# Performance work log

Hardware: AMD Instinct MI355X
Metric: run time of the kernel (lower is better)

The kernel has to match this reference:

```python
import jax, jax.numpy as jnp
import numpy as np


def _conv1d_same(x, k):
    # x: [N, L, Cin], k: [K, Cin, Cout] (flax Conv layout), stride 1, SAME padding
    return jax.lax.conv_general_dilated(
        x, k, window_strides=(1,), padding='SAME',
        dimension_numbers=('NWC', 'WIO', 'NWC'))


def setup_inputs() -> dict:
    key = jax.random.key(0)
    ks = jax.random.split(key, 5)
    B, T, L, C, H, OUT = 16, 64, 512, 64, 150, 24
    xs = jax.random.normal(ks[0], (B, T, L, C), jnp.float32)
    # small init scale to keep gates out of saturation
    ki = jax.random.normal(ks[1], (5, C, 3 * H), jnp.float32) * 0.05
    kh = jax.random.normal(ks[2], (5, H, 3 * H), jnp.float32) * 0.05
    W1 = jax.random.normal(ks[3], (H, H), jnp.float32) * 0.08
    b1 = jnp.zeros((H,), jnp.float32)
    W2 = jax.random.normal(ks[4], (H, OUT), jnp.float32) * 0.08
    b2 = jnp.zeros((OUT,), jnp.float32)
    return {"xs": xs, "ki": ki, "kh": kh, "W1": W1, "b1": b1, "W2": W2, "b2": b2}


def reference(xs, ki, kh, W1, b1, W2, b2):
    B, T, L, C = xs.shape
    H = kh.shape[1]
    # input-to-gates conv for all timesteps at once: [B*T, L, C] -> [B, T, L, 3H]
    gates_i = _conv1d_same(xs.reshape(B * T, L, C), ki).reshape(B, T, L, 3 * H)

    def step(h, gi):
        gh = _conv1d_same(h, kh)                      # [B, L, 3H]
        iir, iiz, iin = jnp.split(gi, 3, axis=-1)
        hir, hiz, hin = jnp.split(gh, 3, axis=-1)
        r = jax.nn.sigmoid(iir + hir)
        z = jax.nn.sigmoid(iiz + hiz)
        n = jnp.tanh(iin + r * hin)
        new_h = (1.0 - z) * n + z * h
        return new_h, new_h

    h0 = jnp.zeros((B, L, H), xs.dtype)
    _, hs = jax.lax.scan(step, h0, jnp.moveaxis(gates_i, 1, 0))  # hs: [T, B, L, H]
    last = hs[-1]                                     # out[:, -1, :] -> [B, L, H]
    hdn = last @ W1 + b1
    hdn = hdn * jax.nn.sigmoid(hdn)                   # silu
    out = hdn @ W2 + b2                               # [B, L, 24]
    return jnp.expand_dims(out, axis=-1)              # [B, L, 24, 1]
```

## Files before the change

### kernel.cpp

```cpp
#include <hip/hip_runtime.h>


#define Bn   16
#define Tn   64
#define Ln   512
#define Cn   64
#define Hn   150
#define G3   450
#define SW   160
#define HP   160
#define KCH  25
#define KCX  10
#define Mtot 8192

typedef __bf16 bf16x8 __attribute__((ext_vector_type(8)));
typedef float  f32x4  __attribute__((ext_vector_type(4)));
typedef short  s16x4  __attribute__((ext_vector_type(4)));

__device__ inline short f2bf(float f) {
  unsigned u = __builtin_bit_cast(unsigned, f);
  u += 0x7fffu + ((u >> 16) & 1u);
  return (short)(u >> 16);
}

__global__ __launch_bounds__(256) void pack_weights(const float* __restrict__ ki,
                                                    const float* __restrict__ kh,
                                                    short* __restrict__ Bx,
                                                    short* __restrict__ Bh) {
  int idx = blockIdx.x * 256 + threadIdx.x;
  if (idx < 32 * KCH * 512) {
    int j = idx & 7, lane = (idx >> 3) & 63;
    int rest = idx >> 9;
    int kc = rest % KCH, nt = rest / KCH;
    int quad = lane >> 4, l16 = lane & 15;
    int n = nt * 16 + l16, seg = n / SW, jl = n - seg * SW;
    int kk = kc / 5, jj = (kc - kk * 5) * 32 + quad * 8 + j;
    float v = (seg < 3 && jl < Hn && jj < Hn) ? kh[(kk * Hn + jj) * G3 + seg * Hn + jl] : 0.f;
    Bh[idx] = f2bf(v);
  } else {
    int r = idx - 32 * KCH * 512;
    if (r < 32 * KCX * 512) {
      int j = r & 7, lane = (r >> 3) & 63;
      int rest = r >> 9;
      int kc = rest % KCX, nt = rest / KCX;
      int quad = lane >> 4, l16 = lane & 15;
      int n = nt * 16 + l16, seg = n / SW, jl = n - seg * SW;
      int kk = kc / 2, cc = (kc - kk * 2) * 32 + quad * 8 + j;
      float v = (seg < 3 && jl < Hn) ? ki[(kk * Cn + cc) * G3 + seg * Hn + jl] : 0.f;
      Bx[r] = f2bf(v);
    }
  }
}

__global__ __launch_bounds__(640)
void gru_step(const short* __restrict__ hbin, short* __restrict__ hbout,
              float* __restrict__ hf, const short* __restrict__ Bh,
              const short* __restrict__ Bx, const float* __restrict__ xs, int t) {
  __shared__ short awh[36 * 168];
  __shared__ short awx[36 * 72];
  const int tid = threadIdx.x;
  const int bb  = blockIdx.x >> 4;
  const int l0  = (blockIdx.x & 15) * 32;

  for (int i = tid; i < 36 * 40; i += 640) {
    int r = i / 40, c4 = (i - r * 40) * 4;
    int l = l0 - 2 + r;
    s16x4 v = {0, 0, 0, 0};
    if (l >= 0 && l < Ln) v = *(const s16x4*)&hbin[((size_t)bb * Ln + l) * HP + c4];
    *(s16x4*)&awh[r * 168 + c4] = v;
  }
  for (int i = tid; i < 36 * 16; i += 640) {
    int r = i >> 4, c4 = (i & 15) * 4;
    int l = l0 - 2 + r;
    s16x4 v = {0, 0, 0, 0};
    if (l >= 0 && l < Ln) {
      f32x4 f = *(const f32x4*)&xs[(((size_t)bb * Tn + t) * Ln + l) * Cn + c4];
      v[0] = f2bf(f[0]); v[1] = f2bf(f[1]); v[2] = f2bf(f[2]); v[3] = f2bf(f[3]);
    }
    *(s16x4*)&awx[r * 72 + c4] = v;
  }
  __syncthreads();

  const int lane = tid & 63, w = tid >> 6;
  const int quad = lane >> 4, l16 = lane & 15;

  const short* Bph[3];
  const short* Bpx[3];
#pragma unroll
  for (int g = 0; g < 3; ++g) {
    Bph[g] = Bh + (size_t)(w + 10 * g) * (KCH * 512) + lane * 8;
    Bpx[g] = Bx + (size_t)(w + 10 * g) * (KCX * 512) + lane * 8;
  }
  const int arh = l16 * 168 + quad * 8;
  const int arx = l16 * 72 + quad * 8;

  f32x4 acc[2][3] = {};
  f32x4 axn[2] = {};

  bf16x8 bx[3][3];
#pragma unroll
  for (int s = 0; s < 2; ++s)
#pragma unroll
    for (int g = 0; g < 3; ++g) bx[s][g] = *(const bf16x8*)(Bpx[g] + s * 512);

  bf16x8 bh[4][3];
#pragma unroll
  for (int s = 0; s < 3; ++s)
#pragma unroll
    for (int g = 0; g < 3; ++g) bh[s][g] = *(const bf16x8*)(Bph[g] + s * 512);

#pragma unroll
  for (int kc = 0; kc < KCH; ++kc) {
    const int cur = kc & 3;
    if (kc + 3 < KCH) {
      const int nxt = (kc + 3) & 3;
#pragma unroll
      for (int g = 0; g < 3; ++g)
        bh[nxt][g] = *(const bf16x8*)(Bph[g] + (kc + 3) * 512);
    }
    const int kk = kc / 5, jj = (kc - kk * 5) * 32;
    const short* ar = &awh[arh + kk * 168 + jj];
    bf16x8 a0 = *(const bf16x8*)(ar);
    bf16x8 a1 = *(const bf16x8*)(ar + 16 * 168);
#pragma unroll
    for (int g = 0; g < 3; ++g) {
      acc[0][g] = __builtin_amdgcn_mfma_f32_16x16x32_bf16(a0, bh[cur][g], acc[0][g], 0, 0, 0);
      acc[1][g] = __builtin_amdgcn_mfma_f32_16x16x32_bf16(a1, bh[cur][g], acc[1][g], 0, 0, 0);
    }
  }

#pragma unroll
  for (int kc = 0; kc < KCX; ++kc) {
    const int cur = kc % 3;
    if (kc + 2 < KCX) {
      const int nxt = (kc + 2) % 3;
#pragma unroll
      for (int g = 0; g < 3; ++g)
        bx[nxt][g] = *(const bf16x8*)(Bpx[g] + (kc + 2) * 512);
    }
    const int kk = kc >> 1, jj = (kc & 1) * 32;
    const short* ar = &awx[arx + kk * 72 + jj];
    bf16x8 a0 = *(const bf16x8*)(ar);
    bf16x8 a1 = *(const bf16x8*)(ar + 16 * 72);
    acc[0][0] = __builtin_amdgcn_mfma_f32_16x16x32_bf16(a0, bx[cur][0], acc[0][0], 0, 0, 0);
    acc[1][0] = __builtin_amdgcn_mfma_f32_16x16x32_bf16(a1, bx[cur][0], acc[1][0], 0, 0, 0);
    acc[0][1] = __builtin_amdgcn_mfma_f32_16x16x32_bf16(a0, bx[cur][1], acc[0][1], 0, 0, 0);
    acc[1][1] = __builtin_amdgcn_mfma_f32_16x16x32_bf16(a1, bx[cur][1], acc[1][1], 0, 0, 0);
    axn[0]    = __builtin_amdgcn_mfma_f32_16x16x32_bf16(a0, bx[cur][2], axn[0], 0, 0, 0);
    axn[1]    = __builtin_amdgcn_mfma_f32_16x16x32_bf16(a1, bx[cur][2], axn[1], 0, 0, 0);
  }

  const int j = w * 16 + l16;
  if (j < Hn) {
#pragma unroll
    for (int mi = 0; mi < 2; ++mi)
#pragma unroll
      for (int r = 0; r < 4; ++r) {
        const int ml = mi * 16 + quad * 4 + r;
        const size_t mrow = (size_t)bb * Ln + l0 + ml;
        float rg = 1.f / (1.f + __expf(-acc[mi][0][r]));
        float zg = 1.f / (1.f + __expf(-acc[mi][1][r]));
        float xg = axn[mi][r] + rg * acc[mi][2][r];
        xg = fminf(fmaxf(xg, -15.f), 15.f);
        float e = __expf(2.f * xg);
        float n = (e - 1.f) / (e + 1.f);
        float hn = (1.f - zg) * n + zg * hf[mrow * Hn + j];
        hf[mrow * Hn + j] = hn;
        hbout[mrow * HP + j] = f2bf(hn);
      }
  }
}

__global__ __launch_bounds__(256) void head1(const float* __restrict__ hf,
                                             const float* __restrict__ W1,
                                             const float* __restrict__ b1,
                                             float* __restrict__ hdn) {
  int idx = blockIdx.x * 256 + threadIdx.x;
  if (idx >= Mtot * Hn) return;
  int m = idx / Hn, j = idx - m * Hn;
  const float* hr = hf + (size_t)m * Hn;
  float acc = b1[j];
#pragma unroll 10
  for (int i = 0; i < Hn; ++i) acc = fmaf(hr[i], W1[i * Hn + j], acc);
  hdn[idx] = acc / (1.f + __expf(-acc));
}
__global__ __launch_bounds__(256) void head2(const float* __restrict__ hdn,
                                             const float* __restrict__ W2,
                                             const float* __restrict__ b2,
                                             float* __restrict__ out) {
  int idx = blockIdx.x * 256 + threadIdx.x;
  if (idx >= Mtot * 24) return;
  int m = idx / 24, j = idx - m * 24;
  const float* hr = hdn + (size_t)m * Hn;
  float acc = b2[j];
#pragma unroll 10
  for (int i = 0; i < Hn; ++i) acc = fmaf(hr[i], W2[i * 24 + j], acc);
  out[idx] = acc;
}

extern "C" void kernel_launch(void* const* d_in, const int* in_sizes, int n_in,
                              void* d_out, int out_size, void* d_ws, size_t ws_size,
                              hipStream_t stream) {
  const float* xs = (const float*)d_in[0];
  const float* ki = (const float*)d_in[1];
  const float* kh = (const float*)d_in[2];
  const float* W1 = (const float*)d_in[3];
  const float* b1 = (const float*)d_in[4];
  const float* W2 = (const float*)d_in[5];
  const float* b2 = (const float*)d_in[6];
  float* out = (float*)d_out;

  char* p = (char*)d_ws;
  float* hf  = (float*)p; p += (size_t)Mtot * Hn * 4;
  float* hdn = (float*)p; p += (size_t)Mtot * Hn * 4;
  short* hbA = (short*)p; p += (size_t)Mtot * HP * 2;
  short* hbB = (short*)p; p += (size_t)Mtot * HP * 2;
  short* Bh  = (short*)p; p += (size_t)32 * KCH * 512 * 2;
  short* Bx  = (short*)p; p += (size_t)32 * KCX * 512 * 2;

  hipMemsetAsync(hf, 0, (size_t)Mtot * Hn * 4, stream);
  hipMemsetAsync(hbA, 0, (size_t)Mtot * HP * 2 * 2, stream);
  pack_weights<<<(32 * (KCH + KCX) * 512 + 255) / 256, 256, 0, stream>>>(ki, kh, Bx, Bh);

  for (int t = 0; t < Tn; ++t) {
    short* hin  = (t & 1) ? hbB : hbA;
    short* hout = (t & 1) ? hbA : hbB;
    gru_step<<<256, 640, 0, stream>>>(hin, hout, hf, Bh, Bx, xs, t);
  }
  head1<<<(Mtot * Hn + 255) / 256, 256, 0, stream>>>(hf, W1, b1, hdn);
  head2<<<(Mtot * 24 + 255) / 256, 256, 0, stream>>>(hdn, W2, b2, out);
}
```

Measured before the change: 1.292 ms.

## Retile GRU step to 64-row M tiles split across two N halves

Each block now covers 64 sequence positions and half of the gate columns using 5 waves, instead of 32 positions and all columns using 10 waves. Each B-weight fragment loaded from global memory is reused across four M subtiles rather than two, which halves weight traffic per MFMA. The halo tile load is restructured so all global loads are issued into registers before the LDS stores, and the old h values are prefetched before the gate math. The cost is more accumulator registers per thread and a larger shared-memory tile.

```diff
diff --git a/kernel.cpp b/kernel.cpp
--- a/kernel.cpp
+++ b/kernel.cpp
@@ -12,6 +12,7 @@
 #define KCH  25
 #define KCX  10
 #define Mtot 8192
+#define NTH  320
 
 typedef __bf16 bf16x8 __attribute__((ext_vector_type(8)));
 typedef float  f32x4  __attribute__((ext_vector_type(4)));
@@ -52,32 +53,60 @@
   }
 }
 
-__global__ __launch_bounds__(640)
+__global__ __launch_bounds__(NTH)
 void gru_step(const short* __restrict__ hbin, short* __restrict__ hbout,
               float* __restrict__ hf, const short* __restrict__ Bh,
               const short* __restrict__ Bx, const float* __restrict__ xs, int t) {
-  __shared__ short awh[36 * 168];
-  __shared__ short awx[36 * 72];
+  __shared__ short awh[68 * 168];
+  __shared__ short awx[68 * 72];
   const int tid = threadIdx.x;
-  const int bb  = blockIdx.x >> 4;
-  const int l0  = (blockIdx.x & 15) * 32;
-
-  for (int i = tid; i < 36 * 40; i += 640) {
-    int r = i / 40, c4 = (i - r * 40) * 4;
-    int l = l0 - 2 + r;
-    s16x4 v = {0, 0, 0, 0};
-    if (l >= 0 && l < Ln) v = *(const s16x4*)&hbin[((size_t)bb * Ln + l) * HP + c4];
-    *(s16x4*)&awh[r * 168 + c4] = v;
-  }
-  for (int i = tid; i < 36 * 16; i += 640) {
-    int r = i >> 4, c4 = (i & 15) * 4;
-    int l = l0 - 2 + r;
-    s16x4 v = {0, 0, 0, 0};
-    if (l >= 0 && l < Ln) {
-      f32x4 f = *(const f32x4*)&xs[(((size_t)bb * Tn + t) * Ln + l) * Cn + c4];
-      v[0] = f2bf(f[0]); v[1] = f2bf(f[1]); v[2] = f2bf(f[2]); v[3] = f2bf(f[3]);
-    }
-    *(s16x4*)&awx[r * 72 + c4] = v;
+  const int ns  = blockIdx.x & 1;
+  const int mb  = blockIdx.x >> 1;
+  const int bb  = mb >> 3;
+  const int l0  = (mb & 7) << 6;
+
+  {
+    s16x4 th[9];
+#pragma unroll
+    for (int u = 0; u < 9; ++u) {
+      int i = tid + u * NTH;
+      int r = i / 40, c4 = (i - r * 40) * 4;
+      int l = l0 - 2 + r;
+      s16x4 v = {0, 0, 0, 0};
+      if (i < 2720 && l >= 0 && l < Ln)
+        v = *(const s16x4*)&hbin[((size_t)bb * Ln + l) * HP + c4];
+      th[u] = v;
+    }
+    f32x4 tx[4];
+#pragma unroll
+    for (int u = 0; u < 4; ++u) {
+      int i = tid + u * NTH;
+      int r = i >> 4, c4 = (i & 15) * 4;
+      int l = l0 - 2 + r;
+      f32x4 f = {0.f, 0.f, 0.f, 0.f};
+      if (i < 1088 && l >= 0 && l < Ln)
+        f = *(const f32x4*)&xs[(((size_t)bb * Tn + t) * Ln + l) * Cn + c4];
+      tx[u] = f;
+    }
+#pragma unroll
+    for (int u = 0; u < 9; ++u) {
+      int i = tid + u * NTH;
+      if (i < 2720) {
+        int r = i / 40, c4 = (i - r * 40) * 4;
+        *(s16x4*)&awh[r * 168 + c4] = th[u];
+      }
+    }
+#pragma unroll
+    for (int u = 0; u < 4; ++u) {
+      int i = tid + u * NTH;
+      if (i < 1088) {
+        int r = i >> 4, c4 = (i & 15) * 4;
+        s16x4 v;
+        v[0] = f2bf(tx[u][0]); v[1] = f2bf(tx[u][1]);
+        v[2] = f2bf(tx[u][2]); v[3] = f2bf(tx[u][3]);
+        *(s16x4*)&awx[r * 72 + c4] = v;
+      }
+    }
   }
   __syncthreads();
 
@@ -88,22 +117,18 @@
   const short* Bpx[3];
 #pragma unroll
   for (int g = 0; g < 3; ++g) {
-    Bph[g] = Bh + (size_t)(w + 10 * g) * (KCH * 512) + lane * 8;
-    Bpx[g] = Bx + (size_t)(w + 10 * g) * (KCX * 512) + lane * 8;
+    const int nt = ns * 5 + w + 10 * g;
+    Bph[g] = Bh + (size_t)nt * (KCH * 512) + lane * 8;
+    Bpx[g] = Bx + (size_t)nt * (KCX * 512) + lane * 8;
   }
   const int arh = l16 * 168 + quad * 8;
   const int arx = l16 * 72 + quad * 8;
 
-  f32x4 acc[2][3] = {};
-  f32x4 axn[2] = {};
-
+  f32x4 acc[4][3] = {};
+  f32x4 axn[4] = {};
+
+  bf16x8 bh[4][3];
   bf16x8 bx[3][3];
-#pragma unroll
-  for (int s = 0; s < 2; ++s)
-#pragma unroll
-    for (int g = 0; g < 3; ++g) bx[s][g] = *(const bf16x8*)(Bpx[g] + s * 512);
-
-  bf16x8 bh[4][3];
 #pragma unroll
   for (int s = 0; s < 3; ++s)
 #pragma unroll
@@ -118,14 +143,26 @@
       for (int g = 0; g < 3; ++g)
         bh[nxt][g] = *(const bf16x8*)(Bph[g] + (kc + 3) * 512);
     }
+    if (kc == KCH - 3) {
+#pragma unroll
+      for (int g = 0; g < 3; ++g) bx[0][g] = *(const bf16x8*)(Bpx[g]);
+    }
+    if (kc == KCH - 2) {
+#pragma unroll
+      for (int g = 0; g < 3; ++g) bx[1][g] = *(const bf16x8*)(Bpx[g] + 512);
+    }
     const int kk = kc / 5, jj = (kc - kk * 5) * 32;
     const short* ar = &awh[arh + kk * 168 + jj];
     bf16x8 a0 = *(const bf16x8*)(ar);
     bf16x8 a1 = *(const bf16x8*)(ar + 16 * 168);
+    bf16x8 a2 = *(const bf16x8*)(ar + 32 * 168);
+    bf16x8 a3 = *(const bf16x8*)(ar + 48 * 168);
 #pragma unroll
     for (int g = 0; g < 3; ++g) {
       acc[0][g] = __builtin_amdgcn_mfma_f32_16x16x32_bf16(a0, bh[cur][g], acc[0][g], 0, 0, 0);
       acc[1][g] = __builtin_amdgcn_mfma_f32_16x16x32_bf16(a1, bh[cur][g], acc[1][g], 0, 0, 0);
+      acc[2][g] = __builtin_amdgcn_mfma_f32_16x16x32_bf16(a2, bh[cur][g], acc[2][g], 0, 0, 0);
+      acc[3][g] = __builtin_amdgcn_mfma_f32_16x16x32_bf16(a3, bh[cur][g], acc[3][g], 0, 0, 0);
     }
   }
 
@@ -142,29 +179,41 @@
     const short* ar = &awx[arx + kk * 72 + jj];
     bf16x8 a0 = *(const bf16x8*)(ar);
     bf16x8 a1 = *(const bf16x8*)(ar + 16 * 72);
-    acc[0][0] = __builtin_amdgcn_mfma_f32_16x16x32_bf16(a0, bx[cur][0], acc[0][0], 0, 0, 0);
-    acc[1][0] = __builtin_amdgcn_mfma_f32_16x16x32_bf16(a1, bx[cur][0], acc[1][0], 0, 0, 0);
-    acc[0][1] = __builtin_amdgcn_mfma_f32_16x16x32_bf16(a0, bx[cur][1], acc[0][1], 0, 0, 0);
-    acc[1][1] = __builtin_amdgcn_mfma_f32_16x16x32_bf16(a1, bx[cur][1], acc[1][1], 0, 0, 0);
-    axn[0]    = __builtin_amdgcn_mfma_f32_16x16x32_bf16(a0, bx[cur][2], axn[0], 0, 0, 0);
-    axn[1]    = __builtin_amdgcn_mfma_f32_16x16x32_bf16(a1, bx[cur][2], axn[1], 0, 0, 0);
-  }
-
-  const int j = w * 16 + l16;
+    bf16x8 a2 = *(const bf16x8*)(ar + 32 * 72);
+    bf16x8 a3 = *(const bf16x8*)(ar + 48 * 72);
+#pragma unroll
+    for (int mi = 0; mi < 4; ++mi) {
+      const bf16x8 am = (mi == 0) ? a0 : (mi == 1) ? a1 : (mi == 2) ? a2 : a3;
+      acc[mi][0] = __builtin_amdgcn_mfma_f32_16x16x32_bf16(am, bx[cur][0], acc[mi][0], 0, 0, 0);
+      acc[mi][1] = __builtin_amdgcn_mfma_f32_16x16x32_bf16(am, bx[cur][1], acc[mi][1], 0, 0, 0);
+      axn[mi]    = __builtin_amdgcn_mfma_f32_16x16x32_bf16(am, bx[cur][2], axn[mi], 0, 0, 0);
+    }
+  }
+
+  const int j = ns * 80 + w * 16 + l16;
   if (j < Hn) {
-#pragma unroll
-    for (int mi = 0; mi < 2; ++mi)
+    const size_t mrow0 = (size_t)bb * Ln + l0;
+    float hold[4][4];
+#pragma unroll
+    for (int mi = 0; mi < 4; ++mi)
 #pragma unroll
       for (int r = 0; r < 4; ++r) {
         const int ml = mi * 16 + quad * 4 + r;
-        const size_t mrow = (size_t)bb * Ln + l0 + ml;
+        hold[mi][r] = hf[(mrow0 + ml) * Hn + j];
+      }
+#pragma unroll
+    for (int mi = 0; mi < 4; ++mi)
+#pragma unroll
+      for (int r = 0; r < 4; ++r) {
+        const int ml = mi * 16 + quad * 4 + r;
+        const size_t mrow = mrow0 + ml;
         float rg = 1.f / (1.f + __expf(-acc[mi][0][r]));
         float zg = 1.f / (1.f + __expf(-acc[mi][1][r]));
         float xg = axn[mi][r] + rg * acc[mi][2][r];
         xg = fminf(fmaxf(xg, -15.f), 15.f);
         float e = __expf(2.f * xg);
         float n = (e - 1.f) / (e + 1.f);
-        float hn = (1.f - zg) * n + zg * hf[mrow * Hn + j];
+        float hn = (1.f - zg) * n + zg * hold[mi][r];
         hf[mrow * Hn + j] = hn;
         hbout[mrow * HP + j] = f2bf(hn);
       }
@@ -225,7 +274,7 @@
   for (int t = 0; t < Tn; ++t) {
     short* hin  = (t & 1) ? hbB : hbA;
     short* hout = (t & 1) ? hbA : hbB;
-    gru_step<<<256, 640, 0, stream>>>(hin, hout, hf, Bh, Bx, xs, t);
+    gru_step<<<256, NTH, 0, stream>>>(hin, hout, hf, Bh, Bx, xs, t);
   }
   head1<<<(Mtot * Hn + 255) / 256, 256, 0, stream>>>(hf, W1, b1, hdn);
   head2<<<(Mtot * 24 + 255) / 256, 256, 0, stream>>>(hdn, W2, b2, out);
```

Measured after the change: 1.618 ms. 25.2% more time.

## Fuse two GRU timesteps per launch using halo recomputation

Applied to the files above, without the earlier changes.

Each launch now advances the recurrence two timesteps. The first step is computed over an extended window of 48 rows, which includes an 8-row halo on each side, and its result is kept in shared memory as the input to the second step. This halves the number of kernel launches and the global round-trips of the hidden state. The cost is redundant halo computation (48 rows instead of 32 in the first step), more shared memory and register pressure, and a mixed precision source for the halo rows of h (bf16 instead of fp32).

```diff
diff --git a/kernel.cpp b/kernel.cpp
--- a/kernel.cpp
+++ b/kernel.cpp
@@ -12,6 +12,7 @@
 #define KCH  25
 #define KCX  10
 #define Mtot 8192
+#define H1S  164
 
 typedef __bf16 bf16x8 __attribute__((ext_vector_type(8)));
 typedef float  f32x4  __attribute__((ext_vector_type(4)));
@@ -21,6 +22,10 @@
   unsigned u = __builtin_bit_cast(unsigned, f);
   u += 0x7fffu + ((u >> 16) & 1u);
   return (short)(u >> 16);
+}
+__device__ inline float bf2f(short s) {
+  unsigned u = ((unsigned)(unsigned short)s) << 16;
+  return __builtin_bit_cast(float, u);
 }
 
 __global__ __launch_bounds__(256) void pack_weights(const float* __restrict__ ki,
@@ -53,36 +58,54 @@
 }
 
 __global__ __launch_bounds__(640)
-void gru_step(const short* __restrict__ hbin, short* __restrict__ hbout,
+void gru_pair(const short* __restrict__ hbin, short* __restrict__ hbout,
               float* __restrict__ hf, const short* __restrict__ Bh,
               const short* __restrict__ Bx, const float* __restrict__ xs, int t) {
-  __shared__ short awh[36 * 168];
-  __shared__ short awx[36 * 72];
+  __shared__ short awh [52 * 168];
+  __shared__ short awh2[36 * 168];
+  __shared__ short awx [52 * 72];
+  __shared__ short awx2[36 * 72];
+  __shared__ float h1l [32 * H1S];
   const int tid = threadIdx.x;
   const int bb  = blockIdx.x >> 4;
-  const int l0  = (blockIdx.x & 15) * 32;
-
-  for (int i = tid; i < 36 * 40; i += 640) {
+  const int l0  = (blockIdx.x & 15) << 5;
+
+  for (int i = tid; i < 52 * 40; i += 640) {
     int r = i / 40, c4 = (i - r * 40) * 4;
-    int l = l0 - 2 + r;
+    int l = l0 - 10 + r;
     s16x4 v = {0, 0, 0, 0};
     if (l >= 0 && l < Ln) v = *(const s16x4*)&hbin[((size_t)bb * Ln + l) * HP + c4];
     *(s16x4*)&awh[r * 168 + c4] = v;
+  }
+  for (int i = tid; i < 52 * 16; i += 640) {
+    int r = i >> 4, c4 = (i & 15) * 4;
+    int l = l0 - 10 + r;
+    s16x4 v = {0, 0, 0, 0};
+    if (l >= 0 && l < Ln) {
+      f32x4 f = *(const f32x4*)&xs[(((size_t)bb * Tn + t) * Ln + l) * Cn + c4];
+      v[0] = f2bf(f[0]); v[1] = f2bf(f[1]); v[2] = f2bf(f[2]); v[3] = f2bf(f[3]);
+    }
+    *(s16x4*)&awx[r * 72 + c4] = v;
   }
   for (int i = tid; i < 36 * 16; i += 640) {
     int r = i >> 4, c4 = (i & 15) * 4;
     int l = l0 - 2 + r;
     s16x4 v = {0, 0, 0, 0};
     if (l >= 0 && l < Ln) {
-      f32x4 f = *(const f32x4*)&xs[(((size_t)bb * Tn + t) * Ln + l) * Cn + c4];
+      f32x4 f = *(const f32x4*)&xs[(((size_t)bb * Tn + t + 1) * Ln + l) * Cn + c4];
       v[0] = f2bf(f[0]); v[1] = f2bf(f[1]); v[2] = f2bf(f[2]); v[3] = f2bf(f[3]);
     }
-    *(s16x4*)&awx[r * 72 + c4] = v;
+    *(s16x4*)&awx2[r * 72 + c4] = v;
+  }
+  if (tid < 360) {
+    int r = tid / 10, c = tid - r * 10;
+    awh2[r * 168 + 150 + c] = 0;
   }
   __syncthreads();
 
   const int lane = tid & 63, w = tid >> 6;
   const int quad = lane >> 4, l16 = lane & 15;
+  const int j = w * 16 + l16;
 
   const short* Bph[3];
   const short* Bpx[3];
@@ -94,79 +117,170 @@
   const int arh = l16 * 168 + quad * 8;
   const int arx = l16 * 72 + quad * 8;
 
-  f32x4 acc[2][3] = {};
-  f32x4 axn[2] = {};
-
-  bf16x8 bx[3][3];
-#pragma unroll
-  for (int s = 0; s < 2; ++s)
-#pragma unroll
-    for (int g = 0; g < 3; ++g) bx[s][g] = *(const bf16x8*)(Bpx[g] + s * 512);
-
-  bf16x8 bh[4][3];
-#pragma unroll
-  for (int s = 0; s < 3; ++s)
-#pragma unroll
-    for (int g = 0; g < 3; ++g) bh[s][g] = *(const bf16x8*)(Bph[g] + s * 512);
-
-#pragma unroll
-  for (int kc = 0; kc < KCH; ++kc) {
-    const int cur = kc & 3;
-    if (kc + 3 < KCH) {
-      const int nxt = (kc + 3) & 3;
-#pragma unroll
-      for (int g = 0; g < 3; ++g)
-        bh[nxt][g] = *(const bf16x8*)(Bph[g] + (kc + 3) * 512);
-    }
-    const int kk = kc / 5, jj = (kc - kk * 5) * 32;
-    const short* ar = &awh[arh + kk * 168 + jj];
-    bf16x8 a0 = *(const bf16x8*)(ar);
-    bf16x8 a1 = *(const bf16x8*)(ar + 16 * 168);
-#pragma unroll
-    for (int g = 0; g < 3; ++g) {
-      acc[0][g] = __builtin_amdgcn_mfma_f32_16x16x32_bf16(a0, bh[cur][g], acc[0][g], 0, 0, 0);
-      acc[1][g] = __builtin_amdgcn_mfma_f32_16x16x32_bf16(a1, bh[cur][g], acc[1][g], 0, 0, 0);
-    }
-  }
-
-#pragma unroll
-  for (int kc = 0; kc < KCX; ++kc) {
-    const int cur = kc % 3;
-    if (kc + 2 < KCX) {
-      const int nxt = (kc + 2) % 3;
-#pragma unroll
-      for (int g = 0; g < 3; ++g)
-        bx[nxt][g] = *(const bf16x8*)(Bpx[g] + (kc + 2) * 512);
-    }
-    const int kk = kc >> 1, jj = (kc & 1) * 32;
-    const short* ar = &awx[arx + kk * 72 + jj];
-    bf16x8 a0 = *(const bf16x8*)(ar);
-    bf16x8 a1 = *(const bf16x8*)(ar + 16 * 72);
-    acc[0][0] = __builtin_amdgcn_mfma_f32_16x16x32_bf16(a0, bx[cur][0], acc[0][0], 0, 0, 0);
-    acc[1][0] = __builtin_amdgcn_mfma_f32_16x16x32_bf16(a1, bx[cur][0], acc[1][0], 0, 0, 0);
-    acc[0][1] = __builtin_amdgcn_mfma_f32_16x16x32_bf16(a0, bx[cur][1], acc[0][1], 0, 0, 0);
-    acc[1][1] = __builtin_amdgcn_mfma_f32_16x16x32_bf16(a1, bx[cur][1], acc[1][1], 0, 0, 0);
-    axn[0]    = __builtin_amdgcn_mfma_f32_16x16x32_bf16(a0, bx[cur][2], axn[0], 0, 0, 0);
-    axn[1]    = __builtin_amdgcn_mfma_f32_16x16x32_bf16(a1, bx[cur][2], axn[1], 0, 0, 0);
-  }
-
-  const int j = w * 16 + l16;
+  f32x4 acc[3][3] = {};
+  f32x4 axn[3] = {};
+  {
+    bf16x8 bh[3][3], bx[3][3];
+#pragma unroll
+    for (int s = 0; s < 2; ++s)
+#pragma unroll
+      for (int g = 0; g < 3; ++g) bh[s][g] = *(const bf16x8*)(Bph[g] + s * 512);
+
+#pragma unroll
+    for (int kc = 0; kc < KCH; ++kc) {
+      const int cur = kc % 3;
+      if (kc + 2 < KCH) {
+        const int nxt = (kc + 2) % 3;
+#pragma unroll
+        for (int g = 0; g < 3; ++g)
+          bh[nxt][g] = *(const bf16x8*)(Bph[g] + (kc + 2) * 512);
+      }
+      if (kc == KCH - 3) {
+#pragma unroll
+        for (int g = 0; g < 3; ++g) bx[0][g] = *(const bf16x8*)(Bpx[g]);
+      }
+      if (kc == KCH - 2) {
+#pragma unroll
+        for (int g = 0; g < 3; ++g) bx[1][g] = *(const bf16x8*)(Bpx[g] + 512);
+      }
+      const int kk = kc / 5, jj = (kc - kk * 5) * 32;
+      const short* ar = &awh[arh + kk * 168 + jj];
+      bf16x8 a0 = *(const bf16x8*)(ar);
+      bf16x8 a1 = *(const bf16x8*)(ar + 16 * 168);
+      bf16x8 a2 = *(const bf16x8*)(ar + 32 * 168);
+#pragma unroll
+      for (int g = 0; g < 3; ++g) {
+        acc[0][g] = __builtin_amdgcn_mfma_f32_16x16x32_bf16(a0, bh[cur][g], acc[0][g], 0, 0, 0);
+        acc[1][g] = __builtin_amdgcn_mfma_f32_16x16x32_bf16(a1, bh[cur][g], acc[1][g], 0, 0, 0);
+        acc[2][g] = __builtin_amdgcn_mfma_f32_16x16x32_bf16(a2, bh[cur][g], acc[2][g], 0, 0, 0);
+      }
+    }
+#pragma unroll
+    for (int kc = 0; kc < KCX; ++kc) {
+      const int cur = kc % 3;
+      if (kc + 2 < KCX) {
+        const int nxt = (kc + 2) % 3;
+#pragma unroll
+        for (int g = 0; g < 3; ++g)
+          bx[nxt][g] = *(const bf16x8*)(Bpx[g] + (kc + 2) * 512);
+      }
+      const int kk = kc >> 1, jj = (kc & 1) * 32;
+      const short* ar = &awx[arx + kk * 72 + jj];
+      bf16x8 a0 = *(const bf16x8*)(ar);
+      bf16x8 a1 = *(const bf16x8*)(ar + 16 * 72);
+      bf16x8 a2 = *(const bf16x8*)(ar + 32 * 72);
+      acc[0][0] = __builtin_amdgcn_mfma_f32_16x16x32_bf16(a0, bx[cur][0], acc[0][0], 0, 0, 0);
+      acc[1][0] = __builtin_amdgcn_mfma_f32_16x16x32_bf16(a1, bx[cur][0], acc[1][0], 0, 0, 0);
+      acc[2][0] = __builtin_amdgcn_mfma_f32_16x16x32_bf16(a2, bx[cur][0], acc[2][0], 0, 0, 0);
+      acc[0][1] = __builtin_amdgcn_mfma_f32_16x16x32_bf16(a0, bx[cur][1], acc[0][1], 0, 0, 0);
+      acc[1][1] = __builtin_amdgcn_mfma_f32_16x16x32_bf16(a1, bx[cur][1], acc[1][1], 0, 0, 0);
+      acc[2][1] = __builtin_amdgcn_mfma_f32_16x16x32_bf16(a2, bx[cur][1], acc[2][1], 0, 0, 0);
+      axn[0]    = __builtin_amdgcn_mfma_f32_16x16x32_bf16(a0, bx[cur][2], axn[0], 0, 0, 0);
+      axn[1]    = __builtin_amdgcn_mfma_f32_16x16x32_bf16(a1, bx[cur][2], axn[1], 0, 0, 0);
+      axn[2]    = __builtin_amdgcn_mfma_f32_16x16x32_bf16(a2, bx[cur][2], axn[2], 0, 0, 0);
+    }
+  }
+
   if (j < Hn) {
 #pragma unroll
-    for (int mi = 0; mi < 2; ++mi)
+    for (int mi = 0; mi < 3; ++mi)
 #pragma unroll
       for (int r = 0; r < 4; ++r) {
-        const int ml = mi * 16 + quad * 4 + r;
-        const size_t mrow = (size_t)bb * Ln + l0 + ml;
+        const int o = mi * 16 + quad * 4 + r;
+        const int l = l0 - 8 + o;
+        const bool own = (o >= 8 && o < 40);
+        float ho;
+        if (own) ho = hf[((size_t)bb * Ln + l) * Hn + j];
+        else     ho = bf2f(awh[(o + 2) * 168 + j]);
         float rg = 1.f / (1.f + __expf(-acc[mi][0][r]));
         float zg = 1.f / (1.f + __expf(-acc[mi][1][r]));
         float xg = axn[mi][r] + rg * acc[mi][2][r];
         xg = fminf(fmaxf(xg, -15.f), 15.f);
         float e = __expf(2.f * xg);
         float n = (e - 1.f) / (e + 1.f);
-        float hn = (1.f - zg) * n + zg * hf[mrow * Hn + j];
-        hf[mrow * Hn + j] = hn;
-        hbout[mrow * HP + j] = f2bf(hn);
+        float h1 = (1.f - zg) * n + zg * ho;
+        if (o >= 6 && o < 42)
+          awh2[(o - 6) * 168 + j] = (l >= 0 && l < Ln) ? f2bf(h1) : (short)0;
+        if (own) h1l[(o - 8) * H1S + j] = h1;
+      }
+  }
+  __syncthreads();
+
+  f32x4 acc2[2][3] = {};
+  f32x4 axn2[2] = {};
+  {
+    bf16x8 bh[3][3], bx[3][3];
+#pragma unroll
+    for (int s = 0; s < 2; ++s)
+#pragma unroll
+      for (int g = 0; g < 3; ++g) bh[s][g] = *(const bf16x8*)(Bph[g] + s * 512);
+
+#pragma unroll
+    for (int kc = 0; kc < KCH; ++kc) {
+      const int cur = kc % 3;
+      if (kc + 2 < KCH) {
+        const int nxt = (kc + 2) % 3;
+#pragma unroll
+        for (int g = 0; g < 3; ++g)
+          bh[nxt][g] = *(const bf16x8*)(Bph[g] + (kc + 2) * 512);
+      }
+      if (kc == KCH - 3) {
+#pragma unroll
+        for (int g = 0; g < 3; ++g) bx[0][g] = *(const bf16x8*)(Bpx[g]);
+      }
+      if (kc == KCH - 2) {
+#pragma unroll
+        for (int g = 0; g < 3; ++g) bx[1][g] = *(const bf16x8*)(Bpx[g] + 512);
+      }
+      const int kk = kc / 5, jj = (kc - kk * 5) * 32;
+      const short* ar = &awh2[arh + kk * 168 + jj];
+      bf16x8 a0 = *(const bf16x8*)(ar);
+      bf16x8 a1 = *(const bf16x8*)(ar + 16 * 168);
+#pragma unroll
+      for (int g = 0; g < 3; ++g) {
+        acc2[0][g] = __builtin_amdgcn_mfma_f32_16x16x32_bf16(a0, bh[cur][g], acc2[0][g], 0, 0, 0);
+        acc2[1][g] = __builtin_amdgcn_mfma_f32_16x16x32_bf16(a1, bh[cur][g], acc2[1][g], 0, 0, 0);
+      }
+    }
+#pragma unroll
+    for (int kc = 0; kc < KCX; ++kc) {
+      const int cur = kc % 3;
+      if (kc + 2 < KCX) {
+        const int nxt = (kc + 2) % 3;
+#pragma unroll
+        for (int g = 0; g < 3; ++g)
+          bx[nxt][g] = *(const bf16x8*)(Bpx[g] + (kc + 2) * 512);
+      }
+      const int kk = kc >> 1, jj = (kc & 1) * 32;
+      const short* ar = &awx2[arx + kk * 72 + jj];
+      bf16x8 a0 = *(const bf16x8*)(ar);
+      bf16x8 a1 = *(const bf16x8*)(ar + 16 * 72);
+      acc2[0][0] = __builtin_amdgcn_mfma_f32_16x16x32_bf16(a0, bx[cur][0], acc2[0][0], 0, 0, 0);
+      acc2[1][0] = __builtin_amdgcn_mfma_f32_16x16x32_bf16(a1, bx[cur][0], acc2[1][0], 0, 0, 0);
+      acc2[0][1] = __builtin_amdgcn_mfma_f32_16x16x32_bf16(a0, bx[cur][1], acc2[0][1], 0, 0, 0);
+      acc2[1][1] = __builtin_amdgcn_mfma_f32_16x16x32_bf16(a1, bx[cur][1], acc2[1][1], 0, 0, 0);
+      axn2[0]    = __builtin_amdgcn_mfma_f32_16x16x32_bf16(a0, bx[cur][2], axn2[0], 0, 0, 0);
+      axn2[1]    = __builtin_amdgcn_mfma_f32_16x16x32_bf16(a1, bx[cur][2], axn2[1], 0, 0, 0);
+    }
+  }
+
+  if (j < Hn) {
+#pragma unroll
+    for (int mi = 0; mi < 2; ++mi)
+#pragma unroll
+      for (int r = 0; r < 4; ++r) {
+        const int o2 = mi * 16 + quad * 4 + r;
+        const size_t mrow = (size_t)bb * Ln + l0 + o2;
+        float ho = h1l[o2 * H1S + j];
+        float rg = 1.f / (1.f + __expf(-acc2[mi][0][r]));
+        float zg = 1.f / (1.f + __expf(-acc2[mi][1][r]));
+        float xg = axn2[mi][r] + rg * acc2[mi][2][r];
+        xg = fminf(fmaxf(xg, -15.f), 15.f);
+        float e = __expf(2.f * xg);
+        float n = (e - 1.f) / (e + 1.f);
+        float h2 = (1.f - zg) * n + zg * ho;
+        hf[mrow * Hn + j] = h2;
+        hbout[mrow * HP + j] = f2bf(h2);
       }
   }
 }
@@ -222,10 +336,10 @@
   hipMemsetAsync(hbA, 0, (size_t)Mtot * HP * 2 * 2, stream);
   pack_weights<<<(32 * (KCH + KCX) * 512 + 255) / 256, 256, 0, stream>>>(ki, kh, Bx, Bh);
 
-  for (int t = 0; t < Tn; ++t) {
-    short* hin  = (t & 1) ? hbB : hbA;
-    short* hout = (t & 1) ? hbA : hbB;
-    gru_step<<<256, 640, 0, stream>>>(hin, hout, hf, Bh, Bx, xs, t);
+  for (int k = 0; k < 32; ++k) {
+    short* hin  = (k & 1) ? hbB : hbA;
+    short* hout = (k & 1) ? hbA : hbB;
+    gru_pair<<<256, 640, 0, stream>>>(hin, hout, hf, Bh, Bx, xs, 2 * k);
   }
   head1<<<(Mtot * Hn + 255) / 256, 256, 0, stream>>>(hf, W1, b1, hdn);
   head2<<<(Mtot * 24 + 255) / 256, 256, 0, stream>>>(hdn, W2, b2, out);
```

Result: slower. 2.252 ms (+74.2%).

## Retile GRU step to 64-row tiles split over two column halves; prefetch old h

Applied to the files above, without the earlier changes.

Each block now covers 64 sequence positions and half of the gate columns (two M-halves times five N-tiles per block) instead of 32 positions and all columns. Weight-fragment reads per block drop to half the columns, and the halo overhead per row shrinks. The LDS staging grows, and the number of blocks stays at 256. The previous fp32 hidden state is also loaded into registers before the input-conv MFMA loop, so its global latency overlaps with that compute.

```diff
diff --git a/kernel.cpp b/kernel.cpp
--- a/kernel.cpp
+++ b/kernel.cpp
@@ -56,20 +56,22 @@
 void gru_step(const short* __restrict__ hbin, short* __restrict__ hbout,
               float* __restrict__ hf, const short* __restrict__ Bh,
               const short* __restrict__ Bx, const float* __restrict__ xs, int t) {
-  __shared__ short awh[36 * 168];
-  __shared__ short awx[36 * 72];
+  __shared__ short awh[68 * 168];
+  __shared__ short awx[68 * 72];
   const int tid = threadIdx.x;
-  const int bb  = blockIdx.x >> 4;
-  const int l0  = (blockIdx.x & 15) * 32;
-
-  for (int i = tid; i < 36 * 40; i += 640) {
+  const int ns  = blockIdx.x & 1;
+  const int mb  = blockIdx.x >> 1;
+  const int bb  = mb >> 3;
+  const int l0  = (mb & 7) << 6;
+
+  for (int i = tid; i < 68 * 40; i += 640) {
     int r = i / 40, c4 = (i - r * 40) * 4;
     int l = l0 - 2 + r;
     s16x4 v = {0, 0, 0, 0};
     if (l >= 0 && l < Ln) v = *(const s16x4*)&hbin[((size_t)bb * Ln + l) * HP + c4];
     *(s16x4*)&awh[r * 168 + c4] = v;
   }
-  for (int i = tid; i < 36 * 16; i += 640) {
+  for (int i = tid; i < 68 * 16; i += 640) {
     int r = i >> 4, c4 = (i & 15) * 4;
     int l = l0 - 2 + r;
     s16x4 v = {0, 0, 0, 0};
@@ -83,16 +85,18 @@
 
   const int lane = tid & 63, w = tid >> 6;
   const int quad = lane >> 4, l16 = lane & 15;
+  const int mh = w / 5, jt = w - mh * 5;
 
   const short* Bph[3];
   const short* Bpx[3];
 #pragma unroll
   for (int g = 0; g < 3; ++g) {
-    Bph[g] = Bh + (size_t)(w + 10 * g) * (KCH * 512) + lane * 8;
-    Bpx[g] = Bx + (size_t)(w + 10 * g) * (KCX * 512) + lane * 8;
-  }
-  const int arh = l16 * 168 + quad * 8;
-  const int arx = l16 * 72 + quad * 8;
+    const int nt = ns * 5 + jt + 10 * g;
+    Bph[g] = Bh + (size_t)nt * (KCH * 512) + lane * 8;
+    Bpx[g] = Bx + (size_t)nt * (KCX * 512) + lane * 8;
+  }
+  const int arh = (mh * 32 + l16) * 168 + quad * 8;
+  const int arx = (mh * 32 + l16) * 72 + quad * 8;
 
   f32x4 acc[2][3] = {};
   f32x4 axn[2] = {};
@@ -127,6 +131,18 @@
       acc[0][g] = __builtin_amdgcn_mfma_f32_16x16x32_bf16(a0, bh[cur][g], acc[0][g], 0, 0, 0);
       acc[1][g] = __builtin_amdgcn_mfma_f32_16x16x32_bf16(a1, bh[cur][g], acc[1][g], 0, 0, 0);
     }
+  }
+
+  const int j = ns * 80 + jt * 16 + l16;
+  float hold[2][4];
+  if (j < Hn) {
+#pragma unroll
+    for (int mi = 0; mi < 2; ++mi)
+#pragma unroll
+      for (int r = 0; r < 4; ++r) {
+        const int ml = mh * 32 + mi * 16 + quad * 4 + r;
+        hold[mi][r] = hf[((size_t)bb * Ln + l0 + ml) * Hn + j];
+      }
   }
 
 #pragma unroll
@@ -150,13 +166,12 @@
     axn[1]    = __builtin_amdgcn_mfma_f32_16x16x32_bf16(a1, bx[cur][2], axn[1], 0, 0, 0);
   }
 
-  const int j = w * 16 + l16;
   if (j < Hn) {
 #pragma unroll
     for (int mi = 0; mi < 2; ++mi)
 #pragma unroll
       for (int r = 0; r < 4; ++r) {
-        const int ml = mi * 16 + quad * 4 + r;
+        const int ml = mh * 32 + mi * 16 + quad * 4 + r;
         const size_t mrow = (size_t)bb * Ln + l0 + ml;
         float rg = 1.f / (1.f + __expf(-acc[mi][0][r]));
         float zg = 1.f / (1.f + __expf(-acc[mi][1][r]));
@@ -164,7 +179,7 @@
         xg = fminf(fmaxf(xg, -15.f), 15.f);
         float e = __expf(2.f * xg);
         float n = (e - 1.f) / (e + 1.f);
-        float hn = (1.f - zg) * n + zg * hf[mrow * Hn + j];
+        float hn = (1.f - zg) * n + zg * hold[mi][r];
         hf[mrow * Hn + j] = hn;
         hbout[mrow * HP + j] = f2bf(hn);
       }
```

Result: slower. 1.457 ms (+12.8%).
